# Kernel tuning notes

Hardware: AMD Instinct MI355X
Metric: run time of the kernel (lower is better)

The kernel has to match this reference:

```python
import jax, jax.numpy as jnp
import numpy as np

B, X, Y, Z, CIN = 4, 64, 64, 64, 32
COUT = 32
MX, MY, MZ = 16, 16, 16


def setup_inputs() -> dict:
    key = jax.random.key(0)
    k1, k2, k3 = jax.random.split(key, 3)
    x = jax.random.normal(k1, (B, X, Y, Z, CIN), dtype=jnp.float32)
    # Glorot-uniform-like scale for (in, out, mx, my, mz) weights
    fan = CIN + COUT
    lim = np.sqrt(6.0 / fan).astype(np.float32)
    w_real = jax.random.uniform(k2, (CIN, COUT, MX, MY, MZ), minval=-lim, maxval=lim, dtype=jnp.float32)
    w_imag = jax.random.uniform(k3, (CIN, COUT, MX, MY, MZ), minval=-lim, maxval=lim, dtype=jnp.float32)
    return {"x": x, "w_real": w_real, "w_imag": w_imag}


def reference(x, w_real, w_imag):
    # tf.signal.fft3d transforms the innermost 3 axes of the 5D input:
    # x is [B, X, Y, Z, C] so the FFT runs over (Y, Z, C) -- faithful to source.
    x_ft = jnp.fft.fftn(x.astype(jnp.complex64), axes=(-3, -2, -1))
    x_ft = jnp.transpose(x_ft, (0, 4, 1, 2, 3))            # [B, C, X, Y, Z]
    mx, my, mz = w_real.shape[2], w_real.shape[3], w_real.shape[4]
    x_crop = x_ft[:, :, :mx, :my, :mz]                     # [B, Cin, mx, my, mz]
    w = jax.lax.complex(w_real, w_imag)                    # [Cin, Cout, mx, my, mz]
    out_ft = jnp.einsum('bixyz,ioxyz->boxyz', x_crop, w)   # [B, Cout, mx, my, mz]
    sx, sy, sz = x.shape[1], x.shape[2], x.shape[3]
    out_ft = jnp.pad(out_ft, ((0, 0), (0, 0), (0, sx - mx), (0, sy - my), (0, sz - mz)))
    out_ft = jnp.transpose(out_ft, (0, 2, 3, 4, 1))        # [B, X, Y, Z, Cout]
    x_out = jnp.fft.ifftn(out_ft, axes=(-3, -2, -1))
    return jnp.real(x_out)
```

## Files before the change

kernel.cpp:

```cpp
#include <hip/hip_runtime.h>
#include <math.h>

#define PI_F 3.14159265358979323846f


__global__ __launch_bounds__(256) void k_dft_z(const float* __restrict__ x,
                                               float2* __restrict__ T1) {
    int bid = blockIdx.x;
    int ih = bid & 1, yg = (bid >> 1) & 7, xx = (bid >> 4) & 15, b = bid >> 8;
    __shared__ float  sx[8192];
    __shared__ float2 twt[1024];
    float4* sx4 = (float4*)sx;
    const float4* src4 = (const float4*)(x + (size_t)((b * 64 + xx) * 64 + yg * 8) * 2048) + ih * 4;
    #pragma unroll
    for (int t = threadIdx.x; t < 2048; t += 256) {
        int i4 = t & 3, z = (t >> 2) & 63, y = t >> 8;
        sx4[(y * 64 + z) * 4 + i4] = src4[(size_t)y * 512 + z * 8 + i4];
    }
    const float cn = -2.0f * PI_F / 64.0f;
    for (int t = threadIdx.x; t < 1024; t += 256) {
        int z = t >> 4, kz = t & 15;
        float s, c; sincosf(cn * (float)((z * kz) & 63), &s, &c);
        twt[t] = make_float2(c, s);
    }
    __syncthreads();
    int ig = threadIdx.x & 3, kz2 = (threadIdx.x >> 2) & 7, y8 = threadIdx.x >> 5;
    float ar0[4], ai0[4], ar1[4], ai1[4];
    #pragma unroll
    for (int j = 0; j < 4; j++) { ar0[j] = ai0[j] = ar1[j] = ai1[j] = 0.f; }
    const float4* twv = (const float4*)twt;
    #pragma unroll 8
    for (int z = 0; z < 64; z++) {
        float4 va = sx4[(y8 * 64 + z) * 4 + ig];
        float4 tp = twv[z * 8 + kz2];
        float v[4] = {va.x, va.y, va.z, va.w};
        #pragma unroll
        for (int j = 0; j < 4; j++) {
            ar0[j] = fmaf(v[j], tp.x, ar0[j]);
            ai0[j] = fmaf(v[j], tp.y, ai0[j]);
            ar1[j] = fmaf(v[j], tp.z, ar1[j]);
            ai1[j] = fmaf(v[j], tp.w, ai1[j]);
        }
    }
    int y = yg * 8 + y8, kz0 = kz2 * 2, i0 = ih * 16 + ig * 4;
    float2* dst = T1 + (size_t)((b * 16 + xx) * 64 + y) * 512;
    float4* d0 = (float4*)(dst + kz0 * 32 + i0);
    d0[0] = make_float4(ar0[0], ai0[0], ar0[1], ai0[1]);
    d0[1] = make_float4(ar0[2], ai0[2], ar0[3], ai0[3]);
    float4* d1 = (float4*)(dst + (kz0 + 1) * 32 + i0);
    d1[0] = make_float4(ar1[0], ai1[0], ar1[1], ai1[1]);
    d1[1] = make_float4(ar1[2], ai1[2], ar1[3], ai1[3]);
}

__global__ __launch_bounds__(256) void k_dft_y(const float2* __restrict__ T1,
                                               float2* __restrict__ XH) {
    int bid = blockIdx.x;
    int ih = bid & 1, kzg = (bid >> 1) & 7, xx = (bid >> 4) & 15, b = bid >> 8;
    __shared__ float4 sT4[2 * 576];
    __shared__ float2 twt[1024];
    const float4* Tg4 = (const float4*)T1;
    size_t gbase = (size_t)(b * 16 + xx) * 64 * 256;
    #pragma unroll
    for (int t = threadIdx.x; t < 1024; t += 256) {
        int i4 = t & 7, kzl = (t >> 3) & 1, y = t >> 4;
        sT4[kzl * 576 + y * 9 + i4] =
            Tg4[gbase + (size_t)y * 256 + (kzg * 2 + kzl) * 16 + ih * 8 + i4];
    }
    const float cn = -2.0f * PI_F / 64.0f;
    for (int t = threadIdx.x; t < 1024; t += 256) {
        int y = t >> 4, ky = t & 15;
        float s, c; sincosf(cn * (float)((y * ky) & 63), &s, &c);
        twt[t] = make_float2(c, s);
    }
    __syncthreads();
    int ig = threadIdx.x & 7, kzl = (threadIdx.x >> 3) & 1, ky = threadIdx.x >> 4;
    float ar0 = 0.f, ai0 = 0.f, ar1 = 0.f, ai1 = 0.f;
    #pragma unroll 8
    for (int y = 0; y < 64; y++) {
        float4 a  = sT4[kzl * 576 + y * 9 + ig];
        float2 tp = twt[y * 16 + ky];
        ar0 += a.x * tp.x - a.y * tp.y;
        ai0 += a.x * tp.y + a.y * tp.x;
        ar1 += a.z * tp.x - a.w * tp.y;
        ai1 += a.z * tp.y + a.w * tp.x;
    }
    int kz = kzg * 2 + kzl;
    float2* dp = XH + (((size_t)(b * 16 + xx) * 16 + ky) * 16 + kz) * 32 + ih * 16 + ig * 2;
    *(float4*)dp = make_float4(ar0, ai0, ar1, ai1);
}

__global__ __launch_bounds__(256) void k_mid(const float2* __restrict__ XH,
                                             const float* __restrict__ wr,
                                             const float* __restrict__ wi,
                                             float2* __restrict__ G) {
    int bid = blockIdx.x;
    int kzq = bid & 3, ky = (bid >> 2) & 15, xx = bid >> 6;
    __shared__ float2 sA[4 * 132];
    __shared__ float2 sB[4 * 192];
    __shared__ float2 twt[1024];
    for (int t = threadIdx.x; t < 512; t += 256) {
        int i = t & 31, kz = (t >> 5) & 3, b = t >> 7;
        sA[b * 132 + kz * 33 + i] =
            XH[(((size_t)(b * 16 + xx) * 16 + ky) * 16 + kzq * 4 + kz) * 32 + i];
    }
    const float cn32 = -2.0f * PI_F / 32.0f;
    for (int t = threadIdx.x; t < 1024; t += 256) {
        int m = t >> 5, k = t & 31;
        float s, c; sincosf(cn32 * (float)((m * k) & 31), &s, &c);
        twt[t] = make_float2(c, s);
    }
    __syncthreads();
    const float4* twv = (const float4*)twt;
    {
        int kz = threadIdx.x & 3, kig = (threadIdx.x >> 2) & 15, b = threadIdx.x >> 6;
        float xr0 = 0.f, xi0 = 0.f, xr1 = 0.f, xi1 = 0.f;
        #pragma unroll 8
        for (int i = 0; i < 32; i++) {
            float2 a  = sA[b * 132 + kz * 33 + i];
            float4 tp = twv[i * 16 + kig];
            xr0 += a.x * tp.x - a.y * tp.y;
            xi0 += a.x * tp.y + a.y * tp.x;
            xr1 += a.x * tp.z - a.y * tp.w;
            xi1 += a.x * tp.w + a.y * tp.z;
        }
        sB[b * 192 + (kig * 2) * 6 + kz]     = make_float2(xr0, xi0);
        sB[b * 192 + (kig * 2 + 1) * 6 + kz] = make_float2(xr1, xi1);
    }
    __syncthreads();
    int o = threadIdx.x & 31, b2 = (threadIdx.x >> 5) & 3, kih = threadIdx.x >> 7;
    float Fr[4], Fi[4];
    {
        #pragma unroll
        for (int q = 0; q < 4; q++) { Fr[q] = Fi[q] = 0.f; }
        const float4* sB4 = (const float4*)sB;
        int wofs = xx * 256 + ky * 16 + kzq * 4;
        #pragma unroll 4
        for (int kk = 0; kk < 16; kk++) {
            int ki = kih * 16 + kk;
            float4 a01 = sB4[b2 * 96 + ki * 3];
            float4 a23 = sB4[b2 * 96 + ki * 3 + 1];
            float4 w4r = *(const float4*)(wr + (size_t)(ki * 32 + o) * 4096 + wofs);
            float4 w4i = *(const float4*)(wi + (size_t)(ki * 32 + o) * 4096 + wofs);
            float xr[4]  = {a01.x, a01.z, a23.x, a23.z};
            float xi[4]  = {a01.y, a01.w, a23.y, a23.w};
            float wrv[4] = {w4r.x, w4r.y, w4r.z, w4r.w};
            float wiv[4] = {w4i.x, w4i.y, w4i.z, w4i.w};
            #pragma unroll
            for (int q = 0; q < 4; q++) {
                Fr[q] += xr[q] * wrv[q] - xi[q] * wiv[q];
                Fi[q] += xr[q] * wiv[q] + xi[q] * wrv[q];
            }
        }
    }
    __syncthreads();
    float2* scratch = sB;
    if (kih == 1) {
        #pragma unroll
        for (int q = 0; q < 4; q++)
            scratch[(b2 * 32 + o) * 4 + q] = make_float2(Fr[q], Fi[q]);
    }
    __syncthreads();
    if (kih == 0) {
        #pragma unroll
        for (int q = 0; q < 4; q++) {
            float2 p = scratch[(b2 * 32 + o) * 4 + q];
            sA[b2 * 132 + q * 33 + o] = make_float2(Fr[q] + p.x, Fi[q] + p.y);
        }
    }
    __syncthreads();
    {
        int kz = threadIdx.x & 3, cog = (threadIdx.x >> 2) & 15, b = threadIdx.x >> 6;
        float gr0 = 0.f, gi0 = 0.f, gr1 = 0.f, gi1 = 0.f;
        #pragma unroll 8
        for (int oo = 0; oo < 32; oo++) {
            float2 f  = sA[b * 132 + kz * 33 + oo];
            float4 tp = twv[oo * 16 + cog];
            gr0 += f.x * tp.x + f.y * tp.y;
            gi0 += f.y * tp.x - f.x * tp.y;
            gr1 += f.x * tp.z + f.y * tp.w;
            gi1 += f.y * tp.z - f.x * tp.w;
        }
        float2* dp = G + (((size_t)(b * 16 + xx) * 16 + ky) * 16 + kzq * 4 + kz) * 32 + cog * 2;
        *(float4*)dp = make_float4(gr0, gi0, gr1, gi1);
    }
}

__global__ __launch_bounds__(256) void k_idft_zy(const float2* __restrict__ G,
                                                 float* __restrict__ out) {
    int bid = blockIdx.x;
    int ch = bid & 1, zc = (bid >> 1) & 7, xx = (bid >> 4) & 63, b = bid >> 10;
    float* dstb = out + (size_t)(b * 64 + xx) * 131072;
    if (xx >= 16) {
        if (ch) return;
        float4* d4 = (float4*)dstb;
        for (int t = threadIdx.x; t < 4096; t += 256) {
            int y = t >> 6, r = t & 63;
            d4[(size_t)y * 512 + zc * 64 + r] = make_float4(0.f, 0.f, 0.f, 0.f);
        }
        return;
    }
    __shared__ float2 sH[128 * 18];
    __shared__ float2 twy[1024];
    __shared__ float2 twz[8 * 17];
    const float cp = 2.0f * PI_F / 64.0f;
    for (int t = threadIdx.x; t < 1024; t += 256) {
        int ky = t >> 6, y = t & 63;
        float s, c; sincosf(cp * (float)((ky * y) & 63), &s, &c);
        twy[t] = make_float2(c, s);
    }
    if (threadIdx.x < 128) {
        int dz = threadIdx.x >> 4, kz = threadIdx.x & 15;
        int z = zc * 8 + dz;
        float s, c; sincosf(cp * (float)((kz * z) & 63), &s, &c);
        twz[dz * 17 + kz] = make_float2(c, s);
    }
    __syncthreads();
    {
        int coq = threadIdx.x & 1, dz = (threadIdx.x >> 1) & 7, ky = threadIdx.x >> 4;
        const float2* Gb = G + ((size_t)(b * 16 + xx) * 16 + ky) * 512 + ch * 16 + coq * 8;
        float Hr[8], Hi[8];
        #pragma unroll
        for (int j = 0; j < 8; j++) { Hr[j] = Hi[j] = 0.f; }
        #pragma unroll 4
        for (int kz = 0; kz < 16; kz++) {
            float2 tz = twz[dz * 17 + kz];
            #pragma unroll
            for (int k = 0; k < 4; k++) {
                float4 g = *(const float4*)(Gb + kz * 32 + k * 2);
                Hr[2 * k]     += g.x * tz.x - g.y * tz.y;
                Hi[2 * k]     += g.x * tz.y + g.y * tz.x;
                Hr[2 * k + 1] += g.z * tz.x - g.w * tz.y;
                Hi[2 * k + 1] += g.z * tz.y + g.w * tz.x;
            }
        }
        float2* hp = sH + (ky * 8 + dz) * 18 + coq * 8;
        #pragma unroll
        for (int k = 0; k < 4; k++)
            *(float4*)(hp + k * 2) = make_float4(Hr[2 * k], Hi[2 * k], Hr[2 * k + 1], Hi[2 * k + 1]);
    }
    __syncthreads();
    {
        int cog = threadIdx.x & 1, dz = (threadIdx.x >> 1) & 7, yg = threadIdx.x >> 4;
        float acc[4][8];
        #pragma unroll
        for (int yl = 0; yl < 4; yl++)
            #pragma unroll
            for (int cl = 0; cl < 8; cl++) acc[yl][cl] = 0.f;
        const float4* twy4 = (const float4*)twy;
        const float4* sH4 = (const float4*)sH;
        for (int ky = 0; ky < 16; ky++) {
            float4 t0 = twy4[ky * 32 + yg * 2 + 0];
            float4 t1 = twy4[ky * 32 + yg * 2 + 1];
            float4 h0 = sH4[(ky * 8 + dz) * 9 + cog * 4 + 0];
            float4 h1 = sH4[(ky * 8 + dz) * 9 + cog * 4 + 1];
            float4 h2 = sH4[(ky * 8 + dz) * 9 + cog * 4 + 2];
            float4 h3 = sH4[(ky * 8 + dz) * 9 + cog * 4 + 3];
            float tc[4] = {t0.x, t0.z, t1.x, t1.z};
            float ts[4] = {t0.y, t0.w, t1.y, t1.w};
            float hr[8] = {h0.x, h0.z, h1.x, h1.z, h2.x, h2.z, h3.x, h3.z};
            float hi[8] = {h0.y, h0.w, h1.y, h1.w, h2.y, h2.w, h3.y, h3.w};
            #pragma unroll
            for (int yl = 0; yl < 4; yl++)
                #pragma unroll
                for (int cl = 0; cl < 8; cl++)
                    acc[yl][cl] += tc[yl] * hr[cl] - ts[yl] * hi[cl];
        }
        const float sc = 1.0f / 131072.0f;
        #pragma unroll
        for (int yl = 0; yl < 4; yl++) {
            int y = yg * 4 + yl;
            float4* d4 = (float4*)(dstb + ((size_t)y * 64 + zc * 8 + dz) * 32 + ch * 16 + cog * 8);
            d4[0] = make_float4(acc[yl][0] * sc, acc[yl][1] * sc, acc[yl][2] * sc, acc[yl][3] * sc);
            d4[1] = make_float4(acc[yl][4] * sc, acc[yl][5] * sc, acc[yl][6] * sc, acc[yl][7] * sc);
        }
    }
}

extern "C" void kernel_launch(void* const* d_in, const int* in_sizes, int n_in,
                              void* d_out, int out_size, void* d_ws, size_t ws_size,
                              hipStream_t stream) {
    const float* x  = (const float*)d_in[0];
    const float* wr = (const float*)d_in[1];
    const float* wi = (const float*)d_in[2];
    float* out = (float*)d_out;
    char*  ws  = (char*)d_ws;
    float2* T1 = (float2*)ws;
    float2* XH = (float2*)(ws + (size_t)16777216);
    float2* Gb = (float2*)(ws + (size_t)16777216 + 4194304);

    k_dft_z  <<<1024, 256, 0, stream>>>(x, T1);
    k_dft_y  <<<1024, 256, 0, stream>>>(T1, XH);
    k_mid    <<<1024, 256, 0, stream>>>(XH, wr, wi, Gb);
    k_idft_zy<<<4096, 256, 0, stream>>>(Gb, out);
}
```

Before: 322.2 us.

## Merge k_mid blocks over all kz and move zero-fill to memset

k_mid now handles all 16 kz per block with 512 threads instead of 4 kz per block. Each thread computes four outputs in the channel DFTs, and the split-K reduction through shared memory with its extra barriers is gone. The zero region of the output (x >= 16) is filled by four hipMemsetAsync calls rather than dedicated blocks of k_idft_zy, so that launch drops to 1024 blocks. The trade-off is fewer, larger k_mid blocks (256), which lowers parallelism, and four added memset launches on the stream.

```diff
diff --git a/kernel.cpp b/kernel.cpp
--- a/kernel.cpp
+++ b/kernel.cpp
@@ -89,22 +89,22 @@
     *(float4*)dp = make_float4(ar0, ai0, ar1, ai1);
 }
 
-__global__ __launch_bounds__(256) void k_mid(const float2* __restrict__ XH,
+__global__ __launch_bounds__(512) void k_mid(const float2* __restrict__ XH,
                                              const float* __restrict__ wr,
                                              const float* __restrict__ wi,
                                              float2* __restrict__ G) {
     int bid = blockIdx.x;
-    int kzq = bid & 3, ky = (bid >> 2) & 15, xx = bid >> 6;
-    __shared__ float2 sA[4 * 132];
-    __shared__ float2 sB[4 * 192];
+    int ky = bid & 15, xx = bid >> 4;
+    __shared__ float2 sA[4 * 528];
+    __shared__ float2 sB[4 * 576];
     __shared__ float2 twt[1024];
-    for (int t = threadIdx.x; t < 512; t += 256) {
-        int i = t & 31, kz = (t >> 5) & 3, b = t >> 7;
-        sA[b * 132 + kz * 33 + i] =
-            XH[(((size_t)(b * 16 + xx) * 16 + ky) * 16 + kzq * 4 + kz) * 32 + i];
+    for (int t = threadIdx.x; t < 2048; t += 512) {
+        int b = t >> 9, kz = (t >> 5) & 15, i = t & 31;
+        sA[b * 528 + kz * 33 + i] =
+            XH[(((size_t)(b * 16 + xx) * 16 + ky) * 16 + kz) * 32 + i];
     }
     const float cn32 = -2.0f * PI_F / 32.0f;
-    for (int t = threadIdx.x; t < 1024; t += 256) {
+    for (int t = threadIdx.x; t < 1024; t += 512) {
         int m = t >> 5, k = t & 31;
         float s, c; sincosf(cn32 * (float)((m * k) & 31), &s, &c);
         twt[t] = make_float2(c, s);
@@ -112,35 +112,38 @@
     __syncthreads();
     const float4* twv = (const float4*)twt;
     {
-        int kz = threadIdx.x & 3, kig = (threadIdx.x >> 2) & 15, b = threadIdx.x >> 6;
-        float xr0 = 0.f, xi0 = 0.f, xr1 = 0.f, xi1 = 0.f;
+        int kz = threadIdx.x & 15, kig = (threadIdx.x >> 4) & 7, b = threadIdx.x >> 7;
+        float xr[4], xi[4];
+        #pragma unroll
+        for (int j = 0; j < 4; j++) { xr[j] = xi[j] = 0.f; }
         #pragma unroll 8
         for (int i = 0; i < 32; i++) {
-            float2 a  = sA[b * 132 + kz * 33 + i];
-            float4 tp = twv[i * 16 + kig];
-            xr0 += a.x * tp.x - a.y * tp.y;
-            xi0 += a.x * tp.y + a.y * tp.x;
-            xr1 += a.x * tp.z - a.y * tp.w;
-            xi1 += a.x * tp.w + a.y * tp.z;
-        }
-        sB[b * 192 + (kig * 2) * 6 + kz]     = make_float2(xr0, xi0);
-        sB[b * 192 + (kig * 2 + 1) * 6 + kz] = make_float2(xr1, xi1);
-    }
-    __syncthreads();
-    int o = threadIdx.x & 31, b2 = (threadIdx.x >> 5) & 3, kih = threadIdx.x >> 7;
-    float Fr[4], Fi[4];
-    {
+            float2 a   = sA[b * 528 + kz * 33 + i];
+            float4 tp0 = twv[i * 16 + kig * 2];
+            float4 tp1 = twv[i * 16 + kig * 2 + 1];
+            xr[0] += a.x * tp0.x - a.y * tp0.y;  xi[0] += a.x * tp0.y + a.y * tp0.x;
+            xr[1] += a.x * tp0.z - a.y * tp0.w;  xi[1] += a.x * tp0.w + a.y * tp0.z;
+            xr[2] += a.x * tp1.x - a.y * tp1.y;  xi[2] += a.x * tp1.y + a.y * tp1.x;
+            xr[3] += a.x * tp1.z - a.y * tp1.w;  xi[3] += a.x * tp1.w + a.y * tp1.z;
+        }
+        #pragma unroll
+        for (int j = 0; j < 4; j++)
+            sB[b * 576 + (kig * 4 + j) * 18 + kz] = make_float2(xr[j], xi[j]);
+    }
+    __syncthreads();
+    {
+        int kzg = threadIdx.x & 3, o = (threadIdx.x >> 2) & 31, b = threadIdx.x >> 7;
+        int wbase = xx * 256 + ky * 16 + kzg * 4;
+        float Fr[4], Fi[4];
         #pragma unroll
         for (int q = 0; q < 4; q++) { Fr[q] = Fi[q] = 0.f; }
         const float4* sB4 = (const float4*)sB;
-        int wofs = xx * 256 + ky * 16 + kzq * 4;
         #pragma unroll 4
-        for (int kk = 0; kk < 16; kk++) {
-            int ki = kih * 16 + kk;
-            float4 a01 = sB4[b2 * 96 + ki * 3];
-            float4 a23 = sB4[b2 * 96 + ki * 3 + 1];
-            float4 w4r = *(const float4*)(wr + (size_t)(ki * 32 + o) * 4096 + wofs);
-            float4 w4i = *(const float4*)(wi + (size_t)(ki * 32 + o) * 4096 + wofs);
+        for (int ki = 0; ki < 32; ki++) {
+            float4 a01 = sB4[b * 288 + ki * 9 + kzg * 2];
+            float4 a23 = sB4[b * 288 + ki * 9 + kzg * 2 + 1];
+            float4 w4r = *(const float4*)(wr + (size_t)(ki * 32 + o) * 4096 + wbase);
+            float4 w4i = *(const float4*)(wi + (size_t)(ki * 32 + o) * 4096 + wbase);
             float xr[4]  = {a01.x, a01.z, a23.x, a23.z};
             float xi[4]  = {a01.y, a01.w, a23.y, a23.w};
             float wrv[4] = {w4r.x, w4r.y, w4r.z, w4r.w};
@@ -151,54 +154,39 @@
                 Fi[q] += xr[q] * wiv[q] + xi[q] * wrv[q];
             }
         }
-    }
-    __syncthreads();
-    float2* scratch = sB;
-    if (kih == 1) {
-        #pragma unroll
-        for (int q = 0; q < 4; q++)
-            scratch[(b2 * 32 + o) * 4 + q] = make_float2(Fr[q], Fi[q]);
-    }
-    __syncthreads();
-    if (kih == 0) {
         #pragma unroll
         for (int q = 0; q < 4; q++) {
-            float2 p = scratch[(b2 * 32 + o) * 4 + q];
-            sA[b2 * 132 + q * 33 + o] = make_float2(Fr[q] + p.x, Fi[q] + p.y);
-        }
-    }
-    __syncthreads();
-    {
-        int kz = threadIdx.x & 3, cog = (threadIdx.x >> 2) & 15, b = threadIdx.x >> 6;
-        float gr0 = 0.f, gi0 = 0.f, gr1 = 0.f, gi1 = 0.f;
+            int kz = kzg * 4 + q;
+            sA[b * 528 + kz * 33 + o] = make_float2(Fr[q], Fi[q]);
+        }
+    }
+    __syncthreads();
+    {
+        int kz = threadIdx.x & 15, cog = (threadIdx.x >> 4) & 7, b = threadIdx.x >> 7;
+        float gr[4], gi[4];
+        #pragma unroll
+        for (int j = 0; j < 4; j++) { gr[j] = gi[j] = 0.f; }
         #pragma unroll 8
-        for (int oo = 0; oo < 32; oo++) {
-            float2 f  = sA[b * 132 + kz * 33 + oo];
-            float4 tp = twv[oo * 16 + cog];
-            gr0 += f.x * tp.x + f.y * tp.y;
-            gi0 += f.y * tp.x - f.x * tp.y;
-            gr1 += f.x * tp.z + f.y * tp.w;
-            gi1 += f.y * tp.z - f.x * tp.w;
-        }
-        float2* dp = G + (((size_t)(b * 16 + xx) * 16 + ky) * 16 + kzq * 4 + kz) * 32 + cog * 2;
-        *(float4*)dp = make_float4(gr0, gi0, gr1, gi1);
+        for (int o = 0; o < 32; o++) {
+            float2 f   = sA[b * 528 + kz * 33 + o];
+            float4 tp0 = twv[o * 16 + cog * 2];
+            float4 tp1 = twv[o * 16 + cog * 2 + 1];
+            gr[0] += f.x * tp0.x + f.y * tp0.y;  gi[0] += f.y * tp0.x - f.x * tp0.y;
+            gr[1] += f.x * tp0.z + f.y * tp0.w;  gi[1] += f.y * tp0.z - f.x * tp0.w;
+            gr[2] += f.x * tp1.x + f.y * tp1.y;  gi[2] += f.y * tp1.x - f.x * tp1.y;
+            gr[3] += f.x * tp1.z + f.y * tp1.w;  gi[3] += f.y * tp1.z - f.x * tp1.w;
+        }
+        float2* dp = G + (((size_t)(b * 16 + xx) * 16 + ky) * 16 + kz) * 32 + cog * 4;
+        ((float4*)dp)[0] = make_float4(gr[0], gi[0], gr[1], gi[1]);
+        ((float4*)dp)[1] = make_float4(gr[2], gi[2], gr[3], gi[3]);
     }
 }
 
 __global__ __launch_bounds__(256) void k_idft_zy(const float2* __restrict__ G,
                                                  float* __restrict__ out) {
     int bid = blockIdx.x;
-    int ch = bid & 1, zc = (bid >> 1) & 7, xx = (bid >> 4) & 63, b = bid >> 10;
+    int ch = bid & 1, zc = (bid >> 1) & 7, xx = (bid >> 4) & 15, b = bid >> 8;
     float* dstb = out + (size_t)(b * 64 + xx) * 131072;
-    if (xx >= 16) {
-        if (ch) return;
-        float4* d4 = (float4*)dstb;
-        for (int t = threadIdx.x; t < 4096; t += 256) {
-            int y = t >> 6, r = t & 63;
-            d4[(size_t)y * 512 + zc * 64 + r] = make_float4(0.f, 0.f, 0.f, 0.f);
-        }
-        return;
-    }
     __shared__ float2 sH[128 * 18];
     __shared__ float2 twy[1024];
     __shared__ float2 twz[8 * 17];
@@ -288,8 +276,12 @@
     float2* XH = (float2*)(ws + (size_t)16777216);
     float2* Gb = (float2*)(ws + (size_t)16777216 + 4194304);
 
+    for (int b = 0; b < 4; ++b)
+        hipMemsetAsync(out + ((size_t)b * 64 + 16) * 131072, 0,
+                       (size_t)48 * 131072 * sizeof(float), stream);
+
     k_dft_z  <<<1024, 256, 0, stream>>>(x, T1);
     k_dft_y  <<<1024, 256, 0, stream>>>(T1, XH);
-    k_mid    <<<1024, 256, 0, stream>>>(XH, wr, wi, Gb);
-    k_idft_zy<<<4096, 256, 0, stream>>>(Gb, out);
-}
+    k_mid    <<< 256, 512, 0, stream>>>(XH, wr, wi, Gb);
+    k_idft_zy<<<1024, 256, 0, stream>>>(Gb, out);
+}
```

New measurement: 308.7 us. -4.2%, faster.
